# Kernel optimization log

Hardware: AMD Instinct MI355X
Metric: run time of the kernel (lower is better)

The kernel has to match this reference:

```python
import jax, jax.numpy as jnp
import numpy as np

B, T, D, U = 32, 4096, 512, 256

def setup_inputs() -> dict:
    key = jax.random.key(0)
    ks = jax.random.split(key, 5)
    s = 1.0 / np.sqrt(D)
    return {
        "values": jax.random.normal(ks[0], (B, T, D), dtype=jnp.float32),
        "query": jax.random.normal(ks[1], (B, D), dtype=jnp.float32),
        "W1": jax.random.normal(ks[2], (D, U), dtype=jnp.float32) * s,
        "b1": jnp.zeros((U,), dtype=jnp.float32),
        "W2": jax.random.normal(ks[3], (D, U), dtype=jnp.float32) * s,
        "b2": jnp.zeros((U,), dtype=jnp.float32),
        "V": jax.random.normal(ks[4], (U, 1), dtype=jnp.float32) * (1.0 / np.sqrt(U)),
        "bV": jnp.zeros((1,), dtype=jnp.float32),
    }

def reference(values, query, W1, b1, W2, b2, V, bV):
    # values: [B,T,D], query: [B,D]
    h_vals = jnp.einsum('btd,du->btu', values, W1) + b1          # [B,T,U]
    h_query = (query @ W2 + b2)[:, None, :]                       # [B,1,U]
    score = jnp.einsum('btu,uo->bto', jnp.tanh(h_vals + h_query), V) + bV  # [B,T,1]
    attention_weights = jax.nn.softmax(score, axis=1)             # [B,T,1]
    context_vector = jnp.sum(attention_weights * values, axis=1)  # [B,D]
    return context_vector, attention_weights
```

## Files before the change

kernel.cpp:

```cpp
#include <hip/hip_runtime.h>
#include <math.h>
#include <stdint.h>

#define BB 32
#define TT 4096
#define DD 512
#define UU 256

#define KC 32
#define NKC (DD/KC)
#define LDA 40
#define NTILE (TT/64)

typedef __attribute__((ext_vector_type(8))) short short8;
typedef __attribute__((ext_vector_type(8))) unsigned short ushort8;
typedef __attribute__((ext_vector_type(4))) float floatx4;

__device__ __forceinline__ unsigned short bf16_rne(float x) {
  union { float f; uint32_t u; } v; v.f = x;
  uint32_t r = v.u + 0x7FFFu + ((v.u >> 16) & 1u);
  return (unsigned short)(r >> 16);
}
__device__ __forceinline__ float tanh_fast(float x) {
  float e = __expf(2.0f * x);
  return 1.0f - 2.0f * __builtin_amdgcn_rcpf(e + 1.0f);
}

#define BAR_LDS()                                     \
  do {                                                \
    asm volatile("s_waitcnt lgkmcnt(0)" ::: "memory");\
    __builtin_amdgcn_s_barrier();                     \
  } while (0)

__global__ __launch_bounds__(256) void setup_kernel(
    const float* __restrict__ W1, unsigned short* __restrict__ w1t,
    const float* __restrict__ query, const float* __restrict__ W2,
    const float* __restrict__ b2, const float* __restrict__ b1,
    float* __restrict__ hq) {
  __shared__ float qs[DD];
  if (blockIdx.x < NKC) {
    const int kc = blockIdx.x;
    const int u = threadIdx.x;
    __attribute__((aligned(16))) unsigned short row[KC];
#pragma unroll
    for (int kk = 0; kk < KC; ++kk)
      row[kk] = bf16_rne(W1[(kc * KC + kk) * UU + u]);
    unsigned short* dst = w1t + ((size_t)kc * UU + u) * KC;
#pragma unroll
    for (int i = 0; i < 4; ++i) ((uint4*)dst)[i] = *(const uint4*)&row[i * 8];
  } else {
    const int b = blockIdx.x - NKC;
    const int u = threadIdx.x;
    for (int d = threadIdx.x; d < DD; d += 256) qs[d] = query[b * DD + d];
    __syncthreads();
    float a0 = 0.f, a1 = 0.f, a2 = 0.f, a3 = 0.f;
#pragma unroll 4
    for (int d = 0; d < DD; d += 4) {
      a0 += qs[d + 0] * W2[(d + 0) * UU + u];
      a1 += qs[d + 1] * W2[(d + 1) * UU + u];
      a2 += qs[d + 2] * W2[(d + 2) * UU + u];
      a3 += qs[d + 3] * W2[(d + 3) * UU + u];
    }
    hq[b * UU + u] = (a0 + a1) + (a2 + a3) + b2[u] + b1[u];
  }
}

__global__ __launch_bounds__(256) void score_kernel(
    const float* __restrict__ values, const unsigned short* __restrict__ w1t,
    const float* __restrict__ hq, const float* __restrict__ V,
    const float* __restrict__ bV, float* __restrict__ scores,
    float* __restrict__ pml, float* __restrict__ pctx) {
  const int b = blockIdx.y;
  const int blk = blockIdx.x;
  const int t0 = blk * 64;
  const int tid = threadIdx.x;
  const int wave = tid >> 6;
  const int lane = tid & 63;
  const int c = lane & 15;
  const int q = lane >> 4;

  __shared__ unsigned short As[2][64 * LDA];
  __shared__ float redW[4][64];
  __shared__ float warr[64];

  floatx4 acc[4][4];
#pragma unroll
  for (int ti = 0; ti < 4; ++ti)
#pragma unroll
    for (int ui = 0; ui < 4; ++ui) acc[ti][ui] = (floatx4){0.f, 0.f, 0.f, 0.f};

  const int ar = tid >> 2;
  const int aseg = tid & 3;
  const float* asrc =
      values + ((size_t)b * TT + t0 + ar) * DD + aseg * 8;

  const unsigned short* bbase = w1t + ((size_t)(wave * 64 + c)) * KC + q * 8;

  float4 aq[2][2];
  short8 bfr[2][4];

  aq[0][0] = *(const float4*)(asrc);
  aq[0][1] = *(const float4*)(asrc + 4);
  aq[1][0] = *(const float4*)(asrc + KC);
  aq[1][1] = *(const float4*)(asrc + KC + 4);
#pragma unroll
  for (int ui = 0; ui < 4; ++ui)
    bfr[0][ui] = *(const short8*)(bbase + (size_t)(ui * 16) * KC);

#pragma unroll
  for (int kc = 0; kc < NKC; ++kc) {
    const int buf = kc & 1;
    {
      const float4 f0 = aq[buf][0], f1 = aq[buf][1];
      ushort8 t8;
      t8[0] = bf16_rne(f0.x); t8[1] = bf16_rne(f0.y);
      t8[2] = bf16_rne(f0.z); t8[3] = bf16_rne(f0.w);
      t8[4] = bf16_rne(f1.x); t8[5] = bf16_rne(f1.y);
      t8[6] = bf16_rne(f1.z); t8[7] = bf16_rne(f1.w);
      *(ushort8*)&As[buf][ar * LDA + aseg * 8] = t8;
    }
    if (kc + 2 < NKC) {
      aq[buf][0] = *(const float4*)(asrc + (kc + 2) * KC);
      aq[buf][1] = *(const float4*)(asrc + (kc + 2) * KC + 4);
    }
    BAR_LDS();
    short8 afr[4];
#pragma unroll
    for (int ti = 0; ti < 4; ++ti)
      afr[ti] = *(const short8*)&As[buf][(ti * 16 + c) * LDA + q * 8];
    if (kc + 1 < NKC) {
#pragma unroll
      for (int ui = 0; ui < 4; ++ui)
        bfr[buf ^ 1][ui] =
            *(const short8*)(bbase + ((size_t)(kc + 1) * UU + ui * 16) * KC);
    }
#pragma unroll
    for (int ti = 0; ti < 4; ++ti)
#pragma unroll
      for (int ui = 0; ui < 4; ++ui)
        acc[ti][ui] = __builtin_amdgcn_mfma_f32_16x16x32_bf16(
            afr[ti], bfr[buf][ui], acc[ti][ui], 0, 0, 0);
  }

  float hqv[4], vv[4];
#pragma unroll
  for (int ui = 0; ui < 4; ++ui) {
    const int u = wave * 64 + ui * 16 + c;
    hqv[ui] = hq[b * UU + u];
    vv[ui] = V[u];
  }
#pragma unroll
  for (int ti = 0; ti < 4; ++ti)
#pragma unroll
    for (int r = 0; r < 4; ++r) {
      float e = 0.0f;
#pragma unroll
      for (int ui = 0; ui < 4; ++ui)
        e += tanh_fast(acc[ti][ui][r] + hqv[ui]) * vv[ui];
      e += __shfl_xor(e, 1, 64);
      e += __shfl_xor(e, 2, 64);
      e += __shfl_xor(e, 4, 64);
      e += __shfl_xor(e, 8, 64);
      if (c == 0) redW[wave][ti * 16 + q * 4 + r] = e;
    }
  __syncthreads();
  if (tid < 64) {
    const float s =
        bV[0] + redW[0][tid] + redW[1][tid] + redW[2][tid] + redW[3][tid];
    scores[b * TT + t0 + tid] = s;
    redW[0][tid] = s;
  }
  __syncthreads();
  float mb = -1e30f;
#pragma unroll 8
  for (int t = 0; t < 64; ++t) mb = fmaxf(mb, redW[0][t]);
  if (tid < 64) warr[tid] = __expf(redW[0][tid] - mb);
  __syncthreads();
  float lb = 0.0f;
#pragma unroll 8
  for (int t = 0; t < 64; ++t) lb += warr[t];

  const float2* vp = (const float2*)(values + ((size_t)b * TT + t0) * DD);
  float2 c2 = {0.f, 0.f};
#pragma unroll 4
  for (int t = 0; t < 64; ++t) {
    const float w = warr[t];
    const float2 v = vp[(size_t)t * (DD / 2) + tid];
    c2.x += w * v.x;
    c2.y += w * v.y;
  }
  *(float2*)&pctx[((size_t)b * NTILE + blk) * DD + 2 * tid] = c2;
  if (tid == 0) {
    pml[(b * NTILE + blk) * 2 + 0] = mb;
    pml[(b * NTILE + blk) * 2 + 1] = lb;
  }
}

__global__ __launch_bounds__(256) void combine_kernel(
    const float* __restrict__ pml, const float* __restrict__ pctx,
    const float* __restrict__ scores, float* __restrict__ out) {
  const int b = blockIdx.x;
  const int tid = threadIdx.x;
  __shared__ float mls[2 * NTILE];
  __shared__ float cs[NTILE];
  if (tid < 2 * NTILE) mls[tid] = pml[b * 2 * NTILE + tid];
  __syncthreads();
  float m = -1e30f;
#pragma unroll 8
  for (int i = 0; i < NTILE; ++i) m = fmaxf(m, mls[2 * i]);
  if (tid < NTILE) cs[tid] = __expf(mls[2 * tid] - m);
  __syncthreads();
  float l = 0.0f;
#pragma unroll 8
  for (int i = 0; i < NTILE; ++i) l += cs[i] * mls[2 * i + 1];
  const float linv = 1.0f / l;

  const float2* pp = (const float2*)(pctx + (size_t)b * NTILE * DD);
  float2 acc = {0.f, 0.f};
#pragma unroll 4
  for (int i = 0; i < NTILE; ++i) {
    const float cw = cs[i];
    const float2 p = pp[(size_t)i * (DD / 2) + tid];
    acc.x += cw * p.x;
    acc.y += cw * p.y;
  }
  out[b * DD + 2 * tid + 0] = acc.x * linv;
  out[b * DD + 2 * tid + 1] = acc.y * linv;

  float* wout = out + BB * DD + (size_t)b * TT;
  const float* srow = scores + (size_t)b * TT;
#pragma unroll
  for (int i = 0; i < TT / 256; ++i) {
    const int t = i * 256 + tid;
    wout[t] = __expf(srow[t] - m) * linv;
  }
}

extern "C" void kernel_launch(void* const* d_in, const int* in_sizes, int n_in,
                              void* d_out, int out_size, void* d_ws, size_t ws_size,
                              hipStream_t stream) {
  const float* values = (const float*)d_in[0];
  const float* query  = (const float*)d_in[1];
  const float* W1     = (const float*)d_in[2];
  const float* b1     = (const float*)d_in[3];
  const float* W2     = (const float*)d_in[4];
  const float* b2     = (const float*)d_in[5];
  const float* V      = (const float*)d_in[6];
  const float* bV     = (const float*)d_in[7];
  float* out = (float*)d_out;

  float* ws = (float*)d_ws;
  float* hq     = ws;
  float* scores = ws + BB * UU;
  float* pml    = scores + BB * TT;
  float* pctx   = pml + BB * NTILE * 2;
  unsigned short* w1t = (unsigned short*)(pctx + (size_t)BB * NTILE * DD);

  setup_kernel<<<NKC + BB, 256, 0, stream>>>(W1, w1t, query, W2, b2, b1, hq);
  score_kernel<<<dim3(NTILE, BB), 256, 0, stream>>>(
      values, w1t, hq, V, bV, scores, pml, pctx);
  combine_kernel<<<BB, 256, 0, stream>>>(pml, pctx, scores, out);
}
```

Baseline: 441.2 us.

## Process two K-chunks per barrier stage with packed bf16 conversion

Restructures the score GEMM main loop so each pipeline stage loads and converts two 32-wide K chunks (64 columns) into a wider LDS tile. This halves the number of barriers and increases the work between them. It also replaces the software bf16 rounding with the hardware v_cvt_pk_bf16_f32 instruction, adds s_setprio around the MFMA blocks, and sets launch bounds to request two blocks per CU. In exchange it uses more registers for the doubled A/B prefetch buffers and more LDS per block, which may reduce occupancy.

```diff
diff --git a/kernel.cpp b/kernel.cpp
--- a/kernel.cpp
+++ b/kernel.cpp
@@ -9,7 +9,8 @@
 
 #define KC 32
 #define NKC (DD/KC)
-#define LDA 40
+#define NST (NKC/2)
+#define LDA2 72
 #define NTILE (TT/64)
 
 typedef __attribute__((ext_vector_type(8))) short short8;
@@ -20,6 +21,11 @@
   union { float f; uint32_t u; } v; v.f = x;
   uint32_t r = v.u + 0x7FFFu + ((v.u >> 16) & 1u);
   return (unsigned short)(r >> 16);
+}
+__device__ __forceinline__ unsigned int cvt_pk_bf16(float a, float b) {
+  unsigned int r;
+  asm("v_cvt_pk_bf16_f32 %0, %1, %2" : "=v"(r) : "v"(a), "v"(b));
+  return r;
 }
 __device__ __forceinline__ float tanh_fast(float x) {
   float e = __expf(2.0f * x);
@@ -65,7 +71,7 @@
   }
 }
 
-__global__ __launch_bounds__(256) void score_kernel(
+__global__ __launch_bounds__(256, 2) void score_kernel(
     const float* __restrict__ values, const unsigned short* __restrict__ w1t,
     const float* __restrict__ hq, const float* __restrict__ V,
     const float* __restrict__ bV, float* __restrict__ scores,
@@ -79,7 +85,7 @@
   const int c = lane & 15;
   const int q = lane >> 4;
 
-  __shared__ unsigned short As[2][64 * LDA];
+  __shared__ unsigned short As[2][64 * LDA2];
   __shared__ float redW[4][64];
   __shared__ float warr[64];
 
@@ -96,50 +102,84 @@
 
   const unsigned short* bbase = w1t + ((size_t)(wave * 64 + c)) * KC + q * 8;
 
-  float4 aq[2][2];
-  short8 bfr[2][4];
-
-  aq[0][0] = *(const float4*)(asrc);
-  aq[0][1] = *(const float4*)(asrc + 4);
-  aq[1][0] = *(const float4*)(asrc + KC);
-  aq[1][1] = *(const float4*)(asrc + KC + 4);
-#pragma unroll
-  for (int ui = 0; ui < 4; ++ui)
-    bfr[0][ui] = *(const short8*)(bbase + (size_t)(ui * 16) * KC);
-
-#pragma unroll
-  for (int kc = 0; kc < NKC; ++kc) {
-    const int buf = kc & 1;
+  float4 aq[2][4];
+  short8 bfr[2][8];
+
+#pragma unroll
+  for (int j = 0; j < 2; ++j) {
+    aq[0][2 * j + 0] = *(const float4*)(asrc + j * KC);
+    aq[0][2 * j + 1] = *(const float4*)(asrc + j * KC + 4);
+    aq[1][2 * j + 0] = *(const float4*)(asrc + (2 + j) * KC);
+    aq[1][2 * j + 1] = *(const float4*)(asrc + (2 + j) * KC + 4);
+  }
+#pragma unroll
+  for (int j = 0; j < 2; ++j)
+#pragma unroll
+    for (int ui = 0; ui < 4; ++ui)
+      bfr[0][j * 4 + ui] =
+          *(const short8*)(bbase + ((size_t)(j * UU) + ui * 16) * KC);
+
+#pragma unroll
+  for (int s = 0; s < NST; ++s) {
+    const int buf = s & 1;
     {
-      const float4 f0 = aq[buf][0], f1 = aq[buf][1];
-      ushort8 t8;
-      t8[0] = bf16_rne(f0.x); t8[1] = bf16_rne(f0.y);
-      t8[2] = bf16_rne(f0.z); t8[3] = bf16_rne(f0.w);
-      t8[4] = bf16_rne(f1.x); t8[5] = bf16_rne(f1.y);
-      t8[6] = bf16_rne(f1.z); t8[7] = bf16_rne(f1.w);
-      *(ushort8*)&As[buf][ar * LDA + aseg * 8] = t8;
-    }
-    if (kc + 2 < NKC) {
-      aq[buf][0] = *(const float4*)(asrc + (kc + 2) * KC);
-      aq[buf][1] = *(const float4*)(asrc + (kc + 2) * KC + 4);
+      uint4 w0, w1;
+      w0.x = cvt_pk_bf16(aq[buf][0].x, aq[buf][0].y);
+      w0.y = cvt_pk_bf16(aq[buf][0].z, aq[buf][0].w);
+      w0.z = cvt_pk_bf16(aq[buf][1].x, aq[buf][1].y);
+      w0.w = cvt_pk_bf16(aq[buf][1].z, aq[buf][1].w);
+      w1.x = cvt_pk_bf16(aq[buf][2].x, aq[buf][2].y);
+      w1.y = cvt_pk_bf16(aq[buf][2].z, aq[buf][2].w);
+      w1.z = cvt_pk_bf16(aq[buf][3].x, aq[buf][3].y);
+      w1.w = cvt_pk_bf16(aq[buf][3].z, aq[buf][3].w);
+      *(uint4*)&As[buf][ar * LDA2 + aseg * 8] = w0;
+      *(uint4*)&As[buf][ar * LDA2 + 32 + aseg * 8] = w1;
+    }
+    if (s + 2 < NST) {
+#pragma unroll
+      for (int j = 0; j < 2; ++j) {
+        aq[buf][2 * j + 0] = *(const float4*)(asrc + (2 * (s + 2) + j) * KC);
+        aq[buf][2 * j + 1] =
+            *(const float4*)(asrc + (2 * (s + 2) + j) * KC + 4);
+      }
     }
     BAR_LDS();
-    short8 afr[4];
-#pragma unroll
-    for (int ti = 0; ti < 4; ++ti)
-      afr[ti] = *(const short8*)&As[buf][(ti * 16 + c) * LDA + q * 8];
-    if (kc + 1 < NKC) {
-#pragma unroll
-      for (int ui = 0; ui < 4; ++ui)
-        bfr[buf ^ 1][ui] =
-            *(const short8*)(bbase + ((size_t)(kc + 1) * UU + ui * 16) * KC);
-    }
-#pragma unroll
-    for (int ti = 0; ti < 4; ++ti)
-#pragma unroll
-      for (int ui = 0; ui < 4; ++ui)
-        acc[ti][ui] = __builtin_amdgcn_mfma_f32_16x16x32_bf16(
-            afr[ti], bfr[buf][ui], acc[ti][ui], 0, 0, 0);
+    if (s + 1 < NST) {
+#pragma unroll
+      for (int j = 0; j < 2; ++j)
+#pragma unroll
+        for (int ui = 0; ui < 4; ++ui)
+          bfr[buf ^ 1][j * 4 + ui] = *(const short8*)(
+              bbase + ((size_t)(2 * (s + 1) + j) * UU + ui * 16) * KC);
+    }
+    {
+      short8 afr[4];
+#pragma unroll
+      for (int ti = 0; ti < 4; ++ti)
+        afr[ti] = *(const short8*)&As[buf][(ti * 16 + c) * LDA2 + q * 8];
+      __builtin_amdgcn_s_setprio(1);
+#pragma unroll
+      for (int ti = 0; ti < 4; ++ti)
+#pragma unroll
+        for (int ui = 0; ui < 4; ++ui)
+          acc[ti][ui] = __builtin_amdgcn_mfma_f32_16x16x32_bf16(
+              afr[ti], bfr[buf][ui], acc[ti][ui], 0, 0, 0);
+      __builtin_amdgcn_s_setprio(0);
+    }
+    {
+      short8 afr[4];
+#pragma unroll
+      for (int ti = 0; ti < 4; ++ti)
+        afr[ti] = *(const short8*)&As[buf][(ti * 16 + c) * LDA2 + 32 + q * 8];
+      __builtin_amdgcn_s_setprio(1);
+#pragma unroll
+      for (int ti = 0; ti < 4; ++ti)
+#pragma unroll
+        for (int ui = 0; ui < 4; ++ui)
+          acc[ti][ui] = __builtin_amdgcn_mfma_f32_16x16x32_bf16(
+              afr[ti], bfr[buf][4 + ui], acc[ti][ui], 0, 0, 0);
+      __builtin_amdgcn_s_setprio(0);
+    }
   }
 
   float hqv[4], vv[4];
```

Result: no change. 434.7 us (median of 2 runs) (-1.5%).
